# Optimization experiments

Measured on AMD Instinct MI355X. Metric: run time of the kernel, lower is better.

Reference implementation:

```python
import jax, jax.numpy as jnp
import numpy as np

EMB = 512       # emb_dim
H = 8           # n_heads
HD = EMB // H   # head_dim = 64
FREQ = 64       # freq_features
PERIOD = 0.1
N = 2048


def setup_inputs() -> dict:
    key = jax.random.key(0)
    ks = jax.random.split(key, 6)
    x = jax.random.normal(ks[0], (1, N, EMB), dtype=jnp.float32)
    v = jax.random.normal(ks[1], (1, N, 3), dtype=jnp.float32)
    vec_map = v / jnp.linalg.norm(v, axis=-1, keepdims=True)  # unit direction vectors
    s_in = 1.0 / np.sqrt(EMB)
    W_qkv = jax.random.normal(ks[2], (EMB, 3 * EMB), dtype=jnp.float32) * s_in
    b_qkv = jnp.zeros((3 * EMB,), dtype=jnp.float32)
    W_bias = jax.random.normal(ks[3], (FREQ, H), dtype=jnp.float32) * (1.0 / np.sqrt(FREQ))
    b_bias = jnp.zeros((H,), dtype=jnp.float32)
    W_out = jax.random.normal(ks[4], (EMB, EMB), dtype=jnp.float32) * s_in
    b_out = jnp.zeros((EMB,), dtype=jnp.float32)
    return {"x": x, "vec_map": vec_map, "W_qkv": W_qkv, "b_qkv": b_qkv,
            "W_bias": W_bias, "b_bias": b_bias, "W_out": W_out, "b_out": b_out}


def reference(x, vec_map, W_qkv, b_qkv, W_bias, b_bias, W_out, b_out):
    batch_dim = x.shape[:-2]
    n = x.shape[-2]
    # QKV projection -> (*, N, H, 3, HD)
    qkv = (x @ W_qkv + b_qkv).reshape(*batch_dim, n, H, 3, HD)
    q, k, v = (qkv[..., 0, :], qkv[..., 1, :], qkv[..., 2, :])
    # attention scores (*, Q, K, H), softmax over the K axis (axis=-2)
    attn = jnp.einsum('...qht,...kht->...qkh', q, k) / np.sqrt(HD)
    attn = jax.nn.softmax(attn, axis=-2)
    # relative bias from pairwise angles between direction vectors
    dot = jnp.einsum('...nc,...mc->...nm', vec_map, vec_map)
    angle = jnp.arccos(jnp.clip(dot, 0.0, 1.0)) / 0.001
    freqs = jnp.linspace(0.0, 1.0, FREQ // 2, dtype=jnp.float32) / PERIOD
    phase = freqs * angle[..., None]                      # (*, N, N, FREQ/2)
    pos = jnp.concatenate((jnp.sin(phase), jnp.cos(phase)), axis=-1)  # (*, N, N, FREQ)
    bias = pos @ W_bias + b_bias                          # (*, N, N, H)
    attn = attn + bias
    # weighted sum of values -> (*, N, EMB)
    y = jnp.einsum('...qkh,...kht->...qht', attn, v).reshape(*batch_dim, n, EMB)
    return y @ W_out + b_out
```

## Files before the change

kernel.cpp:

```cpp
#include <hip/hip_runtime.h>
#include <hip/hip_bf16.h>
#include <math.h>

#define NT 2048
#define EMBD 512
#define NH 8
#define QKV_LD 1536

typedef unsigned short u16;
typedef __attribute__((ext_vector_type(8))) short short8;
typedef __attribute__((ext_vector_type(4))) float v4f;

static __device__ __forceinline__ float bf2f(unsigned int u) {
    union { unsigned int i; float f; } c; c.i = u << 16; return c.f;
}
static __device__ __forceinline__ unsigned int f2bf(float x) {
    union { float f; unsigned int u; } c; c.f = x;
    return (c.u + 0x7fffu + ((c.u >> 16) & 1u)) >> 16;
}

__global__ __launch_bounds__(256) void split_x(const float* __restrict__ x,
    u16* __restrict__ xh, u16* __restrict__ xl)
{
    int i = (blockIdx.x * 256 + threadIdx.x) << 2;
    float4 v = *(const float4*)(x + i);
    float f[4] = {v.x, v.y, v.z, v.w};
    unsigned int hi[4], lo[4];
#pragma unroll
    for (int j = 0; j < 4; ++j) {
        hi[j] = f2bf(f[j]);
        lo[j] = f2bf(f[j] - bf2f(hi[j]));
    }
    uint2 wh; wh.x = hi[0] | (hi[1] << 16); wh.y = hi[2] | (hi[3] << 16);
    uint2 wl; wl.x = lo[0] | (lo[1] << 16); wl.y = lo[2] | (lo[3] << 16);
    *(uint2*)(xh + i) = wh;
    *(uint2*)(xl + i) = wl;
}

__global__ __launch_bounds__(256) void split_wt(const float* __restrict__ W,
    u16* __restrict__ wth, u16* __restrict__ wtl, int ld)
{
    __shared__ float tile[64][65];
    const int n0 = blockIdx.x << 6, k0 = blockIdx.y << 6;
    const int t = threadIdx.x;
    const int r = t >> 2, c4 = (t & 3) << 4;
#pragma unroll
    for (int j = 0; j < 4; ++j)
        *(float4*)&tile[r][c4 + (j << 2)] =
            *(const float4*)(W + (size_t)(k0 + r) * ld + n0 + c4 + (j << 2));
    __syncthreads();
    const int n_l = t >> 2;
    u16 th[16], tl[16];
#pragma unroll
    for (int j = 0; j < 16; ++j) {
        float f = tile[c4 + j][n_l];
        unsigned int h = f2bf(f);
        th[j] = (u16)h;
        tl[j] = (u16)f2bf(f - bf2f(h));
    }
    u16* dh = wth + (size_t)(n0 + n_l) * EMBD + k0 + c4;
    u16* dl = wtl + (size_t)(n0 + n_l) * EMBD + k0 + c4;
    *(uint4*)dh       = *(uint4*)&th[0];
    *(uint4*)(dh + 8) = *(uint4*)&th[8];
    *(uint4*)dl       = *(uint4*)&tl[0];
    *(uint4*)(dl + 8) = *(uint4*)&tl[8];
}

__global__ __launch_bounds__(256) void gemm_qkv_mfma(const u16* __restrict__ xh,
    const u16* __restrict__ xl, const u16* __restrict__ wth,
    const u16* __restrict__ wtl, const float* __restrict__ bias,
    u16* __restrict__ qkvb)
{
    const int n0 = blockIdx.x << 6, m0 = blockIdx.y << 6;
    const int w = threadIdx.x >> 6, lane = threadIdx.x & 63;
    const int wm = w >> 1, wn = w & 1;
    const int fr = lane & 15, kd = (lane >> 4) << 3;

    const u16* ah0 = xh + (size_t)(m0 + wm * 32 + fr) * EMBD + kd;
    const u16* al0 = xl + (size_t)(m0 + wm * 32 + fr) * EMBD + kd;
    const u16* bh0 = wth + (size_t)(n0 + wn * 32 + fr) * EMBD + kd;
    const u16* bl0 = wtl + (size_t)(n0 + wn * 32 + fr) * EMBD + kd;

    v4f acc[2][2] = {};
    for (int kc = 0; kc < EMBD; kc += 32) {
        short8 a_h[2], a_l[2], b_h[2], b_l[2];
#pragma unroll
        for (int im = 0; im < 2; ++im) {
            a_h[im] = *(const short8*)(ah0 + (size_t)im * 16 * EMBD + kc);
            a_l[im] = *(const short8*)(al0 + (size_t)im * 16 * EMBD + kc);
        }
#pragma unroll
        for (int in = 0; in < 2; ++in) {
            b_h[in] = *(const short8*)(bh0 + (size_t)in * 16 * EMBD + kc);
            b_l[in] = *(const short8*)(bl0 + (size_t)in * 16 * EMBD + kc);
        }
#pragma unroll
        for (int im = 0; im < 2; ++im)
#pragma unroll
            for (int in = 0; in < 2; ++in) {
                acc[im][in] = __builtin_amdgcn_mfma_f32_16x16x32_bf16(a_h[im], b_h[in], acc[im][in], 0, 0, 0);
                acc[im][in] = __builtin_amdgcn_mfma_f32_16x16x32_bf16(a_h[im], b_l[in], acc[im][in], 0, 0, 0);
                acc[im][in] = __builtin_amdgcn_mfma_f32_16x16x32_bf16(a_l[im], b_h[in], acc[im][in], 0, 0, 0);
            }
    }
    const int qr = (lane >> 4) << 2;
#pragma unroll
    for (int im = 0; im < 2; ++im)
#pragma unroll
        for (int in = 0; in < 2; ++in) {
            int n = n0 + wn * 32 + in * 16 + fr;
            float bv = bias[n];
#pragma unroll
            for (int r = 0; r < 4; ++r) {
                int m = m0 + wm * 32 + im * 16 + qr + r;
                qkvb[(size_t)m * QKV_LD + n] = (u16)f2bf(acc[im][in][r] + bv);
            }
        }
}

__global__ __launch_bounds__(256) void transpose_v(const u16* __restrict__ qkvb,
                                                   u16* __restrict__ Vt)
{
    __shared__ u16 tile[64][72];
    const int h = blockIdx.y, k0 = blockIdx.x << 6;
    const int t = threadIdx.x;
    {
        int r = t >> 2, cg = (t & 3) << 4;
        const u16* src = qkvb + (size_t)(k0 + r) * QKV_LD + h * 192 + 128 + cg;
        *(uint4*)&tile[r][cg]     = *(const uint4*)src;
        *(uint4*)&tile[r][cg + 8] = *(const uint4*)(src + 8);
    }
    __syncthreads();
    {
        int c = t >> 2, kg = (t & 3) << 4;
        u16 tmp[16];
#pragma unroll
        for (int j = 0; j < 16; ++j) tmp[j] = tile[kg + j][c];
        u16* dst = Vt + ((size_t)h * 64 + c) * NT + k0 + kg;
        *(uint4*)dst       = *(uint4*)&tmp[0];
        *(uint4*)(dst + 8) = *(uint4*)&tmp[8];
    }
}

__global__ __launch_bounds__(256) void flash_attn(const u16* __restrict__ qkvb,
    const u16* __restrict__ Vt, u16* __restrict__ nump,
    float* __restrict__ zpart)
{
    __shared__ u16 P[4][2][16][40];
    const int h = blockIdx.y, z = blockIdx.z;
    const int w = threadIdx.x >> 6, lane = threadIdx.x & 63;
    const int fr = lane & 15, kd = (lane >> 4) << 3, qr = (lane >> 4) << 2;
    const int q0 = (blockIdx.x << 6) + (w << 4);
    const int kbase = z << 9;

    const u16* qb = qkvb + (size_t)(q0 + fr) * QKV_LD + h * 192 + kd;
    short8 qa0 = *(const short8*)(qb);
    short8 qa1 = *(const short8*)(qb + 32);
    const u16* kbp = qkvb + (size_t)kbase * QKV_LD + h * 192 + 64 + kd;
    const u16* vb  = Vt + ((size_t)h * 64 + fr) * NT + kbase + kd;

    v4f acc[4] = {};
    float zac[4] = {};
    int buf = 0;
    for (int kt = 0; kt < 512; kt += 32) {
#pragma unroll
        for (int ks = 0; ks < 2; ++ks) {
            const u16* kr = kbp + (size_t)(kt + ks * 16 + fr) * QKV_LD;
            short8 kb0 = *(const short8*)(kr);
            short8 kb1 = *(const short8*)(kr + 32);
            v4f c = {};
            c = __builtin_amdgcn_mfma_f32_16x16x32_bf16(qa0, kb0, c, 0, 0, 0);
            c = __builtin_amdgcn_mfma_f32_16x16x32_bf16(qa1, kb1, c, 0, 0, 0);
#pragma unroll
            for (int r = 0; r < 4; ++r) {
                float ex = __expf(c[r] * 0.125f);
                zac[r] += ex;
                P[w][buf][qr + r][ks * 16 + fr] = (u16)f2bf(ex);
            }
        }
        union { uint2 u2[2]; short8 s8; } pa;
        pa.u2[0] = *(uint2*)&P[w][buf][fr][kd];
        pa.u2[1] = *(uint2*)&P[w][buf][fr][kd + 4];
#pragma unroll
        for (int ti = 0; ti < 4; ++ti) {
            short8 bfr = *(const short8*)(vb + (size_t)(ti * 16) * NT + kt);
            acc[ti] = __builtin_amdgcn_mfma_f32_16x16x32_bf16(pa.s8, bfr, acc[ti], 0, 0, 0);
        }
        buf ^= 1;
    }
#pragma unroll
    for (int off = 1; off < 16; off <<= 1)
#pragma unroll
        for (int r = 0; r < 4; ++r) zac[r] += __shfl_xor(zac[r], off);
    if (fr == 0) {
#pragma unroll
        for (int r = 0; r < 4; ++r)
            zpart[((size_t)z * NH + h) * NT + q0 + qr + r] = zac[r];
    }
    u16* np = nump + (size_t)z * NT * EMBD;
#pragma unroll
    for (int ti = 0; ti < 4; ++ti)
#pragma unroll
        for (int r = 0; r < 4; ++r)
            np[(size_t)(q0 + qr + r) * EMBD + (h << 6) + (ti << 4) + fr] =
                (u16)f2bf(acc[ti][r]);
}

__global__ __launch_bounds__(256) void bias_mat(const float* __restrict__ vec,
    const float* __restrict__ Wb, const float* __restrict__ bb,
    u16* __restrict__ bm)
{
    __shared__ float flds[32];
    __shared__ float vql[96], vkl[96];
    __shared__ float bbl[8];
    __shared__ float ang_lds[1057];
    __shared__ float biasl[8 * 1057];

    const int t = threadIdx.x;
    int b = blockIdx.x, tq = 0, rem = 64;
    while (b >= rem) { b -= rem; ++tq; --rem; }
    const int tk = tq + b;
    const int q0 = tq << 5, k0 = tk << 5;

    if (t < 32) flds[t] = __fdiv_rn(__fdiv_rn((float)t, 31.0f), 0.1f);
    else if (t < 128) vql[t - 32] = vec[q0 * 3 + (t - 32)];
    else if (t < 224) vkl[t - 128] = vec[k0 * 3 + (t - 128)];
    else if (t < 232) bbl[t - 224] = bb[t - 224];
    __syncthreads();

    {
        const int qq = t & 31, kb = (t >> 5) << 2;
        const float a0 = vql[qq * 3], a1 = vql[qq * 3 + 1], a2 = vql[qq * 3 + 2];
#pragma unroll
        for (int j = 0; j < 4; ++j) {
            const int kk = kb + j;
            float c0 = vkl[kk * 3], c1 = vkl[kk * 3 + 1], c2 = vkl[kk * 3 + 2];
            float dot = __fadd_rn(__fadd_rn(__fmul_rn(a0, c0), __fmul_rn(a1, c1)),
                                  __fmul_rn(a2, c2));
            float dotc = fminf(fmaxf(dot, 0.0f), 1.0f);
            ang_lds[qq * 33 + kk] = __fdiv_rn(acosf(dotc), 0.001f);
        }
    }
    __syncthreads();

    {
        const int w = t >> 6, lane = t & 63;
        const int fr = lane & 15, kd = (lane >> 4) << 3, qr = (lane >> 4) << 2;
        short8 BS, BC;
#pragma unroll
        for (int j = 0; j < 8; ++j) {
            float ws = (fr < 8) ? Wb[(kd + j) * 8 + fr] : 0.0f;
            float wc = (fr < 8) ? Wb[(32 + kd + j) * 8 + fr] : 0.0f;
            BS[j] = (short)f2bf(ws);
            BC[j] = (short)f2bf(wc);
        }
        for (int tt = w; tt < 64; tt += 4) {
            int p = (tt << 4) + fr;
            float ang = ang_lds[(p >> 5) * 33 + (p & 31)];
            short8 AS, AC;
#pragma unroll
            for (int j = 0; j < 8; ++j) {
                float ph = __fmul_rn(flds[kd + j], ang);
                float rv = ph * 0.15915494309189535f;
                float rf = rv - floorf(rv);
                AS[j] = (short)f2bf(__builtin_amdgcn_sinf(rf));
                AC[j] = (short)f2bf(__builtin_amdgcn_cosf(rf));
            }
            v4f c = {};
            c = __builtin_amdgcn_mfma_f32_16x16x32_bf16(AS, BS, c, 0, 0, 0);
            c = __builtin_amdgcn_mfma_f32_16x16x32_bf16(AC, BC, c, 0, 0, 0);
            if (fr < 8) {
#pragma unroll
                for (int r = 0; r < 4; ++r) {
                    int pp = (tt << 4) + qr + r;
                    biasl[fr * 1057 + (pp >> 5) * 33 + (pp & 31)] = c[r];
                }
            }
        }
    }
    __syncthreads();

    const int row = t >> 3, c4 = (t & 7) << 2;
#pragma unroll
    for (int h = 0; h < 8; ++h) {
        const float bv = bbl[h];
        unsigned int o[4];
#pragma unroll
        for (int j = 0; j < 4; ++j)
            o[j] = f2bf(biasl[h * 1057 + row * 33 + c4 + j] + bv);
        uint2 wv; wv.x = o[0] | (o[1] << 16); wv.y = o[2] | (o[3] << 16);
        *(uint2*)(bm + ((size_t)h * NT + q0 + row) * NT + k0 + c4) = wv;
    }
    if (tk != tq) {
#pragma unroll
        for (int h = 0; h < 8; ++h) {
            const float bv = bbl[h];
            unsigned int o[4];
#pragma unroll
            for (int j = 0; j < 4; ++j)
                o[j] = f2bf(biasl[h * 1057 + (c4 + j) * 33 + row] + bv);
            uint2 wv; wv.x = o[0] | (o[1] << 16); wv.y = o[2] | (o[3] << 16);
            *(uint2*)(bm + ((size_t)h * NT + k0 + row) * NT + q0 + c4) = wv;
        }
    }
}

__global__ __launch_bounds__(256) void biasv_mfma(const u16* __restrict__ bm,
    const u16* __restrict__ Vt, float* __restrict__ bpart)
{
    const int h = blockIdx.y, z = blockIdx.z;
    const int q0 = (blockIdx.x << 6) + ((threadIdx.x >> 6) << 4);
    const int lane = threadIdx.x & 63;
    const int fr = lane & 15;
    const int kd = (lane >> 4) << 3;
    const int kbase = z << 10;

    const u16* arow  = bm + (size_t)(h * NT + q0 + fr) * NT + kbase + kd;
    const u16* vbase = Vt + ((size_t)h * 64 + fr) * NT + kbase + kd;

    v4f c[4] = {};
    for (int ks = 0; ks < 1024; ks += 32) {
        short8 a = *(const short8*)(arow + ks);
#pragma unroll
        for (int nt = 0; nt < 4; ++nt) {
            short8 bv = *(const short8*)(vbase + (size_t)nt * 16 * NT + ks);
            c[nt] = __builtin_amdgcn_mfma_f32_16x16x32_bf16(a, bv, c[nt], 0, 0, 0);
        }
    }
    float* bp = bpart + (size_t)z * NT * EMBD;
    const int qr = (lane >> 4) << 2;
#pragma unroll
    for (int nt = 0; nt < 4; ++nt)
#pragma unroll
        for (int r = 0; r < 4; ++r)
            bp[(size_t)(q0 + qr + r) * EMBD + (h << 6) + (nt << 4) + fr] = c[nt][r];
}

__global__ __launch_bounds__(256) void combine_emit(const u16* __restrict__ nump,
    const float* __restrict__ zpart, const float* __restrict__ bpart,
    u16* __restrict__ yh, u16* __restrict__ yl)
{
    const int MN = NT * EMBD;
    int i = (blockIdx.x * 256 + threadIdx.x) << 2;
    const int q = i >> 9, h = (i & 511) >> 6;
    float zs = 0.f;
#pragma unroll
    for (int z = 0; z < 4; ++z) zs += zpart[((size_t)z * NH + h) * NT + q];
    const float inv = 1.0f / zs;
    float a[4] = {};
#pragma unroll
    for (int z = 0; z < 4; ++z) {
        uint2 r = *(const uint2*)(nump + (size_t)z * MN + i);
        a[0] += bf2f(r.x & 0xffffu); a[1] += bf2f(r.x >> 16);
        a[2] += bf2f(r.y & 0xffffu); a[3] += bf2f(r.y >> 16);
    }
    float bsum[4] = {};
#pragma unroll
    for (int z = 0; z < 2; ++z) {
        float4 p = *(const float4*)(bpart + (size_t)z * MN + i);
        bsum[0] += p.x; bsum[1] += p.y; bsum[2] += p.z; bsum[3] += p.w;
    }
    unsigned int hi[4], lo[4];
#pragma unroll
    for (int j = 0; j < 4; ++j) {
        float y = a[j] * inv + bsum[j];
        hi[j] = f2bf(y);
        lo[j] = f2bf(y - bf2f(hi[j]));
    }
    uint2 wh; wh.x = hi[0] | (hi[1] << 16); wh.y = hi[2] | (hi[3] << 16);
    uint2 wl; wl.x = lo[0] | (lo[1] << 16); wl.y = lo[2] | (lo[3] << 16);
    *(uint2*)(yh + i) = wh;
    *(uint2*)(yl + i) = wl;
}

__global__ __launch_bounds__(256) void gemm_out_mfma(const u16* __restrict__ yh,
    const u16* __restrict__ yl, const u16* __restrict__ wh,
    const u16* __restrict__ wl, const float* __restrict__ bias,
    float* __restrict__ out)
{
    const int n0 = blockIdx.x << 6, m0 = blockIdx.y << 6;
    const int w = threadIdx.x >> 6, lane = threadIdx.x & 63;
    const int wm = w >> 1, wn = w & 1;
    const int fr = lane & 15, kd = (lane >> 4) << 3;

    const u16* ah0 = yh + (size_t)(m0 + wm * 32 + fr) * EMBD + kd;
    const u16* al0 = yl + (size_t)(m0 + wm * 32 + fr) * EMBD + kd;
    const u16* bh0 = wh + (size_t)(n0 + wn * 32 + fr) * EMBD + kd;
    const u16* bl0 = wl + (size_t)(n0 + wn * 32 + fr) * EMBD + kd;

    v4f acc[2][2] = {};
    for (int kc = 0; kc < EMBD; kc += 32) {
        short8 a_h[2], a_l[2], b_h[2], b_l[2];
#pragma unroll
        for (int im = 0; im < 2; ++im) {
            a_h[im] = *(const short8*)(ah0 + (size_t)im * 16 * EMBD + kc);
            a_l[im] = *(const short8*)(al0 + (size_t)im * 16 * EMBD + kc);
        }
#pragma unroll
        for (int in = 0; in < 2; ++in) {
            b_h[in] = *(const short8*)(bh0 + (size_t)in * 16 * EMBD + kc);
            b_l[in] = *(const short8*)(bl0 + (size_t)in * 16 * EMBD + kc);
        }
#pragma unroll
        for (int im = 0; im < 2; ++im)
#pragma unroll
            for (int in = 0; in < 2; ++in) {
                acc[im][in] = __builtin_amdgcn_mfma_f32_16x16x32_bf16(a_h[im], b_h[in], acc[im][in], 0, 0, 0);
                acc[im][in] = __builtin_amdgcn_mfma_f32_16x16x32_bf16(a_h[im], b_l[in], acc[im][in], 0, 0, 0);
                acc[im][in] = __builtin_amdgcn_mfma_f32_16x16x32_bf16(a_l[im], b_h[in], acc[im][in], 0, 0, 0);
            }
    }
    const int qr = (lane >> 4) << 2;
#pragma unroll
    for (int im = 0; im < 2; ++im)
#pragma unroll
        for (int in = 0; in < 2; ++in) {
            int n = n0 + wn * 32 + in * 16 + fr;
            float bv = bias[n];
#pragma unroll
            for (int r = 0; r < 4; ++r) {
                int m = m0 + wm * 32 + im * 16 + qr + r;
                out[(size_t)m * EMBD + n] = acc[im][in][r] + bv;
            }
        }
}

extern "C" void kernel_launch(void* const* d_in, const int* in_sizes, int n_in,
                              void* d_out, int out_size, void* d_ws, size_t ws_size,
                              hipStream_t stream)
{
    const float* x    = (const float*)d_in[0];
    const float* vec  = (const float*)d_in[1];
    const float* Wqkv = (const float*)d_in[2];
    const float* bqkv = (const float*)d_in[3];
    const float* Wb   = (const float*)d_in[4];
    const float* bb   = (const float*)d_in[5];
    const float* Wout = (const float*)d_in[6];
    const float* bout = (const float*)d_in[7];
    float* out = (float*)d_out;

    char* ws = (char*)d_ws;
    u16*   qkvb  = (u16*)(ws);
    u16*   Vt    = (u16*)(ws + 6291456);
    float* zpart = (float*)(ws + 8388608);
    u16*   nump  = (u16*)(ws + 8650752);
    float* bpart = (float*)(ws + 17039360);
    u16*   yh    = (u16*)(ws + 25427968);
    u16*   yl    = (u16*)(ws + 27525120);
    u16*   bm    = (u16*)(ws + 29622272);
    u16*   xh    = (u16*)(ws + 29622272);
    u16*   xl    = (u16*)(ws + 31719424);
    u16*   wth   = (u16*)(ws + 33816576);
    u16*   wtl   = (u16*)(ws + 35389440);
    u16*   woth  = (u16*)(ws + 29622272);
    u16*   wotl  = (u16*)(ws + 30146560);

    split_x<<<1024, 256, 0, stream>>>(x, xh, xl);
    split_wt<<<dim3(24, 8), 256, 0, stream>>>(Wqkv, wth, wtl, QKV_LD);
    gemm_qkv_mfma<<<dim3(24, 32), 256, 0, stream>>>(xh, xl, wth, wtl, bqkv, qkvb);
    transpose_v<<<dim3(32, 8), 256, 0, stream>>>(qkvb, Vt);
    flash_attn<<<dim3(32, 8, 4), 256, 0, stream>>>(qkvb, Vt, nump, zpart);
    bias_mat<<<2080, 256, 0, stream>>>(vec, Wb, bb, bm);
    biasv_mfma<<<dim3(32, 8, 2), 256, 0, stream>>>(bm, Vt, bpart);
    combine_emit<<<1024, 256, 0, stream>>>(nump, zpart, bpart, yh, yl);
    split_wt<<<dim3(8, 8), 256, 0, stream>>>(Wout, woth, wotl, EMBD);
    gemm_out_mfma<<<dim3(8, 32), 256, 0, stream>>>(yh, yl, woth, wotl, bout, out);
}
```

Baseline: 283.8 us.

## Merge prep kernels, split flash attention over more key chunks, prefetch K

Folds the x split and both weight split/transposes into one prep launch, removing two kernel launches. Flash attention now splits keys into 8 chunks of 256 instead of 4 of 512, doubling grid parallelism, and prefetches the next K tile while using a single P buffer. The bias-times-V kernel is unrolled to two MFMAs per step. The workspace is reorganised so nump aliases the big scratch region after bias_mat/biasv finish, which is why flash_attn is reordered after biasv. In exchange, combine_emit reads twice as many partial sums.

```diff
diff --git a/kernel.cpp b/kernel.cpp
--- a/kernel.cpp
+++ b/kernel.cpp
@@ -19,30 +19,10 @@
     return (c.u + 0x7fffu + ((c.u >> 16) & 1u)) >> 16;
 }
 
-__global__ __launch_bounds__(256) void split_x(const float* __restrict__ x,
-    u16* __restrict__ xh, u16* __restrict__ xl)
-{
-    int i = (blockIdx.x * 256 + threadIdx.x) << 2;
-    float4 v = *(const float4*)(x + i);
-    float f[4] = {v.x, v.y, v.z, v.w};
-    unsigned int hi[4], lo[4];
-#pragma unroll
-    for (int j = 0; j < 4; ++j) {
-        hi[j] = f2bf(f[j]);
-        lo[j] = f2bf(f[j] - bf2f(hi[j]));
-    }
-    uint2 wh; wh.x = hi[0] | (hi[1] << 16); wh.y = hi[2] | (hi[3] << 16);
-    uint2 wl; wl.x = lo[0] | (lo[1] << 16); wl.y = lo[2] | (lo[3] << 16);
-    *(uint2*)(xh + i) = wh;
-    *(uint2*)(xl + i) = wl;
-}
-
-__global__ __launch_bounds__(256) void split_wt(const float* __restrict__ W,
-    u16* __restrict__ wth, u16* __restrict__ wtl, int ld)
+static __device__ __forceinline__ void split_wt_tile(const float* __restrict__ W,
+    u16* __restrict__ wth, u16* __restrict__ wtl, int ld, int n0, int k0, int t)
 {
     __shared__ float tile[64][65];
-    const int n0 = blockIdx.x << 6, k0 = blockIdx.y << 6;
-    const int t = threadIdx.x;
     const int r = t >> 2, c4 = (t & 3) << 4;
 #pragma unroll
     for (int j = 0; j < 4; ++j)
@@ -64,6 +44,36 @@
     *(uint4*)(dh + 8) = *(uint4*)&th[8];
     *(uint4*)dl       = *(uint4*)&tl[0];
     *(uint4*)(dl + 8) = *(uint4*)&tl[8];
+}
+
+__global__ __launch_bounds__(256) void prep(const float* __restrict__ x,
+    const float* __restrict__ Wqkv, const float* __restrict__ Wout,
+    u16* __restrict__ xh, u16* __restrict__ xl,
+    u16* __restrict__ wth, u16* __restrict__ wtl,
+    u16* __restrict__ woth, u16* __restrict__ wotl)
+{
+    const int b = blockIdx.x, t = threadIdx.x;
+    if (b < 1024) {
+        int i = (b * 256 + t) << 2;
+        float4 v = *(const float4*)(x + i);
+        float f[4] = {v.x, v.y, v.z, v.w};
+        unsigned int hi[4], lo[4];
+#pragma unroll
+        for (int j = 0; j < 4; ++j) {
+            hi[j] = f2bf(f[j]);
+            lo[j] = f2bf(f[j] - bf2f(hi[j]));
+        }
+        uint2 wh; wh.x = hi[0] | (hi[1] << 16); wh.y = hi[2] | (hi[3] << 16);
+        uint2 wl; wl.x = lo[0] | (lo[1] << 16); wl.y = lo[2] | (lo[3] << 16);
+        *(uint2*)(xh + i) = wh;
+        *(uint2*)(xl + i) = wl;
+    } else if (b < 1216) {
+        int bb = b - 1024;
+        split_wt_tile(Wqkv, wth, wtl, QKV_LD, (bb % 24) << 6, (bb / 24) << 6, t);
+    } else {
+        int bb = b - 1216;
+        split_wt_tile(Wout, woth, wotl, EMBD, (bb & 7) << 6, (bb >> 3) << 6, t);
+    }
 }
 
 __global__ __launch_bounds__(256) void gemm_qkv_mfma(const u16* __restrict__ xh,
@@ -142,70 +152,6 @@
     }
 }
 
-__global__ __launch_bounds__(256) void flash_attn(const u16* __restrict__ qkvb,
-    const u16* __restrict__ Vt, u16* __restrict__ nump,
-    float* __restrict__ zpart)
-{
-    __shared__ u16 P[4][2][16][40];
-    const int h = blockIdx.y, z = blockIdx.z;
-    const int w = threadIdx.x >> 6, lane = threadIdx.x & 63;
-    const int fr = lane & 15, kd = (lane >> 4) << 3, qr = (lane >> 4) << 2;
-    const int q0 = (blockIdx.x << 6) + (w << 4);
-    const int kbase = z << 9;
-
-    const u16* qb = qkvb + (size_t)(q0 + fr) * QKV_LD + h * 192 + kd;
-    short8 qa0 = *(const short8*)(qb);
-    short8 qa1 = *(const short8*)(qb + 32);
-    const u16* kbp = qkvb + (size_t)kbase * QKV_LD + h * 192 + 64 + kd;
-    const u16* vb  = Vt + ((size_t)h * 64 + fr) * NT + kbase + kd;
-
-    v4f acc[4] = {};
-    float zac[4] = {};
-    int buf = 0;
-    for (int kt = 0; kt < 512; kt += 32) {
-#pragma unroll
-        for (int ks = 0; ks < 2; ++ks) {
-            const u16* kr = kbp + (size_t)(kt + ks * 16 + fr) * QKV_LD;
-            short8 kb0 = *(const short8*)(kr);
-            short8 kb1 = *(const short8*)(kr + 32);
-            v4f c = {};
-            c = __builtin_amdgcn_mfma_f32_16x16x32_bf16(qa0, kb0, c, 0, 0, 0);
-            c = __builtin_amdgcn_mfma_f32_16x16x32_bf16(qa1, kb1, c, 0, 0, 0);
-#pragma unroll
-            for (int r = 0; r < 4; ++r) {
-                float ex = __expf(c[r] * 0.125f);
-                zac[r] += ex;
-                P[w][buf][qr + r][ks * 16 + fr] = (u16)f2bf(ex);
-            }
-        }
-        union { uint2 u2[2]; short8 s8; } pa;
-        pa.u2[0] = *(uint2*)&P[w][buf][fr][kd];
-        pa.u2[1] = *(uint2*)&P[w][buf][fr][kd + 4];
-#pragma unroll
-        for (int ti = 0; ti < 4; ++ti) {
-            short8 bfr = *(const short8*)(vb + (size_t)(ti * 16) * NT + kt);
-            acc[ti] = __builtin_amdgcn_mfma_f32_16x16x32_bf16(pa.s8, bfr, acc[ti], 0, 0, 0);
-        }
-        buf ^= 1;
-    }
-#pragma unroll
-    for (int off = 1; off < 16; off <<= 1)
-#pragma unroll
-        for (int r = 0; r < 4; ++r) zac[r] += __shfl_xor(zac[r], off);
-    if (fr == 0) {
-#pragma unroll
-        for (int r = 0; r < 4; ++r)
-            zpart[((size_t)z * NH + h) * NT + q0 + qr + r] = zac[r];
-    }
-    u16* np = nump + (size_t)z * NT * EMBD;
-#pragma unroll
-    for (int ti = 0; ti < 4; ++ti)
-#pragma unroll
-        for (int r = 0; r < 4; ++r)
-            np[(size_t)(q0 + qr + r) * EMBD + (h << 6) + (ti << 4) + fr] =
-                (u16)f2bf(acc[ti][r]);
-}
-
 __global__ __launch_bounds__(256) void bias_mat(const float* __restrict__ vec,
     const float* __restrict__ Wb, const float* __restrict__ bb,
     u16* __restrict__ bm)
@@ -319,12 +265,15 @@
     const u16* vbase = Vt + ((size_t)h * 64 + fr) * NT + kbase + kd;
 
     v4f c[4] = {};
-    for (int ks = 0; ks < 1024; ks += 32) {
-        short8 a = *(const short8*)(arow + ks);
+    for (int ks = 0; ks < 1024; ks += 64) {
+        short8 a0 = *(const short8*)(arow + ks);
+        short8 a1 = *(const short8*)(arow + ks + 32);
 #pragma unroll
         for (int nt = 0; nt < 4; ++nt) {
-            short8 bv = *(const short8*)(vbase + (size_t)nt * 16 * NT + ks);
-            c[nt] = __builtin_amdgcn_mfma_f32_16x16x32_bf16(a, bv, c[nt], 0, 0, 0);
+            short8 b0 = *(const short8*)(vbase + (size_t)nt * 16 * NT + ks);
+            short8 b1 = *(const short8*)(vbase + (size_t)nt * 16 * NT + ks + 32);
+            c[nt] = __builtin_amdgcn_mfma_f32_16x16x32_bf16(a0, b0, c[nt], 0, 0, 0);
+            c[nt] = __builtin_amdgcn_mfma_f32_16x16x32_bf16(a1, b1, c[nt], 0, 0, 0);
         }
     }
     float* bp = bpart + (size_t)z * NT * EMBD;
@@ -334,6 +283,83 @@
 #pragma unroll
         for (int r = 0; r < 4; ++r)
             bp[(size_t)(q0 + qr + r) * EMBD + (h << 6) + (nt << 4) + fr] = c[nt][r];
+}
+
+__global__ __launch_bounds__(256) void flash_attn(const u16* __restrict__ qkvb,
+    const u16* __restrict__ Vt, u16* __restrict__ nump,
+    float* __restrict__ zpart)
+{
+    __shared__ u16 P[4][16][40];
+    const int h = blockIdx.y, z = blockIdx.z;
+    const int w = threadIdx.x >> 6, lane = threadIdx.x & 63;
+    const int fr = lane & 15, kd = (lane >> 4) << 3, qr = (lane >> 4) << 2;
+    const int q0 = (blockIdx.x << 6) + (w << 4);
+    const int kbase = z << 8;
+
+    const u16* qb = qkvb + (size_t)(q0 + fr) * QKV_LD + h * 192 + kd;
+    short8 qa0 = *(const short8*)(qb);
+    short8 qa1 = *(const short8*)(qb + 32);
+    const u16* kbp = qkvb + (size_t)kbase * QKV_LD + h * 192 + 64 + kd;
+    const u16* vb  = Vt + ((size_t)h * 64 + fr) * NT + kbase + kd;
+
+    short8 k0a, k0b, k1a, k1b;
+    {
+        const u16* kr0 = kbp + (size_t)fr * QKV_LD;
+        const u16* kr1 = kbp + (size_t)(16 + fr) * QKV_LD;
+        k0a = *(const short8*)(kr0); k0b = *(const short8*)(kr0 + 32);
+        k1a = *(const short8*)(kr1); k1b = *(const short8*)(kr1 + 32);
+    }
+    v4f acc[4] = {};
+    float zac[4] = {};
+    for (int kt = 0; kt < 256; kt += 32) {
+        short8 ck0a = k0a, ck0b = k0b, ck1a = k1a, ck1b = k1b;
+        if (kt + 32 < 256) {
+            const u16* kr0 = kbp + (size_t)(kt + 32 + fr) * QKV_LD;
+            const u16* kr1 = kbp + (size_t)(kt + 48 + fr) * QKV_LD;
+            k0a = *(const short8*)(kr0); k0b = *(const short8*)(kr0 + 32);
+            k1a = *(const short8*)(kr1); k1b = *(const short8*)(kr1 + 32);
+        }
+        short8 v0 = *(const short8*)(vb + (size_t)0 * 16 * NT + kt);
+        short8 v1 = *(const short8*)(vb + (size_t)1 * 16 * NT + kt);
+        short8 v2 = *(const short8*)(vb + (size_t)2 * 16 * NT + kt);
+        short8 v3 = *(const short8*)(vb + (size_t)3 * 16 * NT + kt);
+        v4f c0 = {}, c1 = {};
+        c0 = __builtin_amdgcn_mfma_f32_16x16x32_bf16(qa0, ck0a, c0, 0, 0, 0);
+        c0 = __builtin_amdgcn_mfma_f32_16x16x32_bf16(qa1, ck0b, c0, 0, 0, 0);
+        c1 = __builtin_amdgcn_mfma_f32_16x16x32_bf16(qa0, ck1a, c1, 0, 0, 0);
+        c1 = __builtin_amdgcn_mfma_f32_16x16x32_bf16(qa1, ck1b, c1, 0, 0, 0);
+#pragma unroll
+        for (int r = 0; r < 4; ++r) {
+            float e0 = __expf(c0[r] * 0.125f);
+            float e1 = __expf(c1[r] * 0.125f);
+            zac[r] += e0 + e1;
+            P[w][qr + r][fr]      = (u16)f2bf(e0);
+            P[w][qr + r][16 + fr] = (u16)f2bf(e1);
+        }
+        union { uint2 u2[2]; short8 s8; } pa;
+        pa.u2[0] = *(uint2*)&P[w][fr][kd];
+        pa.u2[1] = *(uint2*)&P[w][fr][kd + 4];
+        acc[0] = __builtin_amdgcn_mfma_f32_16x16x32_bf16(pa.s8, v0, acc[0], 0, 0, 0);
+        acc[1] = __builtin_amdgcn_mfma_f32_16x16x32_bf16(pa.s8, v1, acc[1], 0, 0, 0);
+        acc[2] = __builtin_amdgcn_mfma_f32_16x16x32_bf16(pa.s8, v2, acc[2], 0, 0, 0);
+        acc[3] = __builtin_amdgcn_mfma_f32_16x16x32_bf16(pa.s8, v3, acc[3], 0, 0, 0);
+    }
+#pragma unroll
+    for (int off = 1; off < 16; off <<= 1)
+#pragma unroll
+        for (int r = 0; r < 4; ++r) zac[r] += __shfl_xor(zac[r], off);
+    if (fr == 0) {
+#pragma unroll
+        for (int r = 0; r < 4; ++r)
+            zpart[((size_t)z * NH + h) * NT + q0 + qr + r] = zac[r];
+    }
+    u16* np = nump + (size_t)z * NT * EMBD;
+#pragma unroll
+    for (int ti = 0; ti < 4; ++ti)
+#pragma unroll
+        for (int r = 0; r < 4; ++r)
+            np[(size_t)(q0 + qr + r) * EMBD + (h << 6) + (ti << 4) + fr] =
+                (u16)f2bf(acc[ti][r]);
 }
 
 __global__ __launch_bounds__(256) void combine_emit(const u16* __restrict__ nump,
@@ -345,11 +371,11 @@
     const int q = i >> 9, h = (i & 511) >> 6;
     float zs = 0.f;
 #pragma unroll
-    for (int z = 0; z < 4; ++z) zs += zpart[((size_t)z * NH + h) * NT + q];
+    for (int z = 0; z < 8; ++z) zs += zpart[((size_t)z * NH + h) * NT + q];
     const float inv = 1.0f / zs;
     float a[4] = {};
 #pragma unroll
-    for (int z = 0; z < 4; ++z) {
+    for (int z = 0; z < 8; ++z) {
         uint2 r = *(const uint2*)(nump + (size_t)z * MN + i);
         a[0] += bf2f(r.x & 0xffffu); a[1] += bf2f(r.x >> 16);
         a[2] += bf2f(r.y & 0xffffu); a[3] += bf2f(r.y >> 16);
@@ -443,26 +469,25 @@
     u16*   qkvb  = (u16*)(ws);
     u16*   Vt    = (u16*)(ws + 6291456);
     float* zpart = (float*)(ws + 8388608);
-    u16*   nump  = (u16*)(ws + 8650752);
-    float* bpart = (float*)(ws + 17039360);
-    u16*   yh    = (u16*)(ws + 25427968);
-    u16*   yl    = (u16*)(ws + 27525120);
-    u16*   bm    = (u16*)(ws + 29622272);
-    u16*   xh    = (u16*)(ws + 29622272);
-    u16*   xl    = (u16*)(ws + 31719424);
-    u16*   wth   = (u16*)(ws + 33816576);
-    u16*   wtl   = (u16*)(ws + 35389440);
-    u16*   woth  = (u16*)(ws + 29622272);
-    u16*   wotl  = (u16*)(ws + 30146560);
-
-    split_x<<<1024, 256, 0, stream>>>(x, xh, xl);
-    split_wt<<<dim3(24, 8), 256, 0, stream>>>(Wqkv, wth, wtl, QKV_LD);
+    float* bpart = (float*)(ws + 8912896);
+    u16*   yh    = (u16*)(ws + 17301504);
+    u16*   yl    = (u16*)(ws + 19398656);
+    u16*   woth  = (u16*)(ws + 21495808);
+    u16*   wotl  = (u16*)(ws + 22020096);
+    char*  big   = ws + 22544384;
+    u16*   xh    = (u16*)(big);
+    u16*   xl    = (u16*)(big + 2097152);
+    u16*   wth   = (u16*)(big + 4194304);
+    u16*   wtl   = (u16*)(big + 5767168);
+    u16*   bm    = (u16*)(big);
+    u16*   nump  = (u16*)(big);
+
+    prep<<<1280, 256, 0, stream>>>(x, Wqkv, Wout, xh, xl, wth, wtl, woth, wotl);
     gemm_qkv_mfma<<<dim3(24, 32), 256, 0, stream>>>(xh, xl, wth, wtl, bqkv, qkvb);
     transpose_v<<<dim3(32, 8), 256, 0, stream>>>(qkvb, Vt);
-    flash_attn<<<dim3(32, 8, 4), 256, 0, stream>>>(qkvb, Vt, nump, zpart);
     bias_mat<<<2080, 256, 0, stream>>>(vec, Wb, bb, bm);
     biasv_mfma<<<dim3(32, 8, 2), 256, 0, stream>>>(bm, Vt, bpart);
+    flash_attn<<<dim3(32, 8, 8), 256, 0, stream>>>(qkvb, Vt, nump, zpart);
     combine_emit<<<1024, 256, 0, stream>>>(nump, zpart, bpart, yh, yl);
-    split_wt<<<dim3(8, 8), 256, 0, stream>>>(Wout, woth, wotl, EMBD);
     gemm_out_mfma<<<dim3(8, 32), 256, 0, stream>>>(yh, yl, woth, wotl, bout, out);
 }
```

Result: no change. 284.4 us (+0.2%).

## Merge prep kernels, fuse V transpose into QKV GEMM, resplit bias-V reduction

Applied to the files above, without the earlier changes.

One prep kernel now splits x, W_qkv and W_out into bf16 hi/lo pairs, replacing three separate launches. The QKV GEMM blocks that produce V tiles stage them in LDS and write the transposed Vt directly, so the standalone transpose kernel is gone. bias_mat stores bf16 into a smaller LDS buffer and folds the bias into the MFMA accumulator init. biasv_mfma now splits K four ways with two MFMAs per step, and combine_emit sums four partials. The workspace is reordered so bm and nump share one buffer, which requires the bias pass to run before flash attention and moves launch order around.

```diff
diff --git a/kernel.cpp b/kernel.cpp
--- a/kernel.cpp
+++ b/kernel.cpp
@@ -19,30 +19,10 @@
     return (c.u + 0x7fffu + ((c.u >> 16) & 1u)) >> 16;
 }
 
-__global__ __launch_bounds__(256) void split_x(const float* __restrict__ x,
-    u16* __restrict__ xh, u16* __restrict__ xl)
-{
-    int i = (blockIdx.x * 256 + threadIdx.x) << 2;
-    float4 v = *(const float4*)(x + i);
-    float f[4] = {v.x, v.y, v.z, v.w};
-    unsigned int hi[4], lo[4];
-#pragma unroll
-    for (int j = 0; j < 4; ++j) {
-        hi[j] = f2bf(f[j]);
-        lo[j] = f2bf(f[j] - bf2f(hi[j]));
-    }
-    uint2 wh; wh.x = hi[0] | (hi[1] << 16); wh.y = hi[2] | (hi[3] << 16);
-    uint2 wl; wl.x = lo[0] | (lo[1] << 16); wl.y = lo[2] | (lo[3] << 16);
-    *(uint2*)(xh + i) = wh;
-    *(uint2*)(xl + i) = wl;
-}
-
-__global__ __launch_bounds__(256) void split_wt(const float* __restrict__ W,
-    u16* __restrict__ wth, u16* __restrict__ wtl, int ld)
+static __device__ __forceinline__ void split_wt_tile(const float* __restrict__ W,
+    u16* __restrict__ wth, u16* __restrict__ wtl, int ld, int n0, int k0, int t)
 {
     __shared__ float tile[64][65];
-    const int n0 = blockIdx.x << 6, k0 = blockIdx.y << 6;
-    const int t = threadIdx.x;
     const int r = t >> 2, c4 = (t & 3) << 4;
 #pragma unroll
     for (int j = 0; j < 4; ++j)
@@ -66,13 +46,46 @@
     *(uint4*)(dl + 8) = *(uint4*)&tl[8];
 }
 
+__global__ __launch_bounds__(256) void prep(const float* __restrict__ x,
+    const float* __restrict__ Wqkv, const float* __restrict__ Wout,
+    u16* __restrict__ xh, u16* __restrict__ xl,
+    u16* __restrict__ wth, u16* __restrict__ wtl,
+    u16* __restrict__ woth, u16* __restrict__ wotl)
+{
+    const int b = blockIdx.x, t = threadIdx.x;
+    if (b < 1024) {
+        int i = (b * 256 + t) << 2;
+        float4 v = *(const float4*)(x + i);
+        float f[4] = {v.x, v.y, v.z, v.w};
+        unsigned int hi[4], lo[4];
+#pragma unroll
+        for (int j = 0; j < 4; ++j) {
+            hi[j] = f2bf(f[j]);
+            lo[j] = f2bf(f[j] - bf2f(hi[j]));
+        }
+        uint2 wh; wh.x = hi[0] | (hi[1] << 16); wh.y = hi[2] | (hi[3] << 16);
+        uint2 wl; wl.x = lo[0] | (lo[1] << 16); wl.y = lo[2] | (lo[3] << 16);
+        *(uint2*)(xh + i) = wh;
+        *(uint2*)(xl + i) = wl;
+    } else if (b < 1216) {
+        int bb = b - 1024;
+        split_wt_tile(Wqkv, wth, wtl, QKV_LD, (bb % 24) << 6, (bb / 24) << 6, t);
+    } else {
+        int bb = b - 1216;
+        split_wt_tile(Wout, woth, wotl, EMBD, (bb & 7) << 6, (bb >> 3) << 6, t);
+    }
+}
+
 __global__ __launch_bounds__(256) void gemm_qkv_mfma(const u16* __restrict__ xh,
     const u16* __restrict__ xl, const u16* __restrict__ wth,
     const u16* __restrict__ wtl, const float* __restrict__ bias,
-    u16* __restrict__ qkvb)
-{
-    const int n0 = blockIdx.x << 6, m0 = blockIdx.y << 6;
-    const int w = threadIdx.x >> 6, lane = threadIdx.x & 63;
+    u16* __restrict__ qkvb, u16* __restrict__ Vt)
+{
+    __shared__ u16 vtile[64][72];
+    const int bn = blockIdx.x;
+    const int n0 = bn << 6, m0 = blockIdx.y << 6;
+    const int t = threadIdx.x;
+    const int w = t >> 6, lane = t & 63;
     const int wm = w >> 1, wn = w & 1;
     const int fr = lane & 15, kd = (lane >> 4) << 3;
 
@@ -104,42 +117,173 @@
             }
     }
     const int qr = (lane >> 4) << 2;
-#pragma unroll
-    for (int im = 0; im < 2; ++im)
-#pragma unroll
-        for (int in = 0; in < 2; ++in) {
-            int n = n0 + wn * 32 + in * 16 + fr;
-            float bv = bias[n];
-#pragma unroll
-            for (int r = 0; r < 4; ++r) {
-                int m = m0 + wm * 32 + im * 16 + qr + r;
-                qkvb[(size_t)m * QKV_LD + n] = (u16)f2bf(acc[im][in][r] + bv);
-            }
-        }
-}
-
-__global__ __launch_bounds__(256) void transpose_v(const u16* __restrict__ qkvb,
-                                                   u16* __restrict__ Vt)
-{
-    __shared__ u16 tile[64][72];
-    const int h = blockIdx.y, k0 = blockIdx.x << 6;
-    const int t = threadIdx.x;
-    {
-        int r = t >> 2, cg = (t & 3) << 4;
-        const u16* src = qkvb + (size_t)(k0 + r) * QKV_LD + h * 192 + 128 + cg;
-        *(uint4*)&tile[r][cg]     = *(const uint4*)src;
-        *(uint4*)&tile[r][cg + 8] = *(const uint4*)(src + 8);
-    }
-    __syncthreads();
-    {
-        int c = t >> 2, kg = (t & 3) << 4;
+    if (bn % 3 != 2) {
+#pragma unroll
+        for (int im = 0; im < 2; ++im)
+#pragma unroll
+            for (int in = 0; in < 2; ++in) {
+                int n = n0 + wn * 32 + in * 16 + fr;
+                float bv = bias[n];
+#pragma unroll
+                for (int r = 0; r < 4; ++r) {
+                    int m = m0 + wm * 32 + im * 16 + qr + r;
+                    qkvb[(size_t)m * QKV_LD + n] = (u16)f2bf(acc[im][in][r] + bv);
+                }
+            }
+    } else {
+        const int h = bn / 3;
+#pragma unroll
+        for (int im = 0; im < 2; ++im)
+#pragma unroll
+            for (int in = 0; in < 2; ++in) {
+                int nl = wn * 32 + in * 16 + fr;
+                float bv = bias[n0 + nl];
+#pragma unroll
+                for (int r = 0; r < 4; ++r)
+                    vtile[wm * 32 + im * 16 + qr + r][nl] =
+                        (u16)f2bf(acc[im][in][r] + bv);
+            }
+        __syncthreads();
+        const int c = t >> 2, kg = (t & 3) << 4;
         u16 tmp[16];
 #pragma unroll
-        for (int j = 0; j < 16; ++j) tmp[j] = tile[kg + j][c];
-        u16* dst = Vt + ((size_t)h * 64 + c) * NT + k0 + kg;
+        for (int j = 0; j < 16; ++j) tmp[j] = vtile[kg + j][c];
+        u16* dst = Vt + ((size_t)h * 64 + c) * NT + m0 + kg;
         *(uint4*)dst       = *(uint4*)&tmp[0];
         *(uint4*)(dst + 8) = *(uint4*)&tmp[8];
     }
+}
+
+__global__ __launch_bounds__(256) void bias_mat(const float* __restrict__ vec,
+    const float* __restrict__ Wb, const float* __restrict__ bb,
+    u16* __restrict__ bm)
+{
+    __shared__ float flds[32];
+    __shared__ float vql[96], vkl[96];
+    __shared__ float bbl[8];
+    __shared__ float ang_lds[1057];
+    __shared__ u16 biaslu[8 * 1057];
+
+    const int t = threadIdx.x;
+    int b = blockIdx.x, tq = 0, rem = 64;
+    while (b >= rem) { b -= rem; ++tq; --rem; }
+    const int tk = tq + b;
+    const int q0 = tq << 5, k0 = tk << 5;
+
+    if (t < 32) flds[t] = __fdiv_rn(__fdiv_rn((float)t, 31.0f), 0.1f);
+    else if (t < 128) vql[t - 32] = vec[q0 * 3 + (t - 32)];
+    else if (t < 224) vkl[t - 128] = vec[k0 * 3 + (t - 128)];
+    else if (t < 232) bbl[t - 224] = bb[t - 224];
+    __syncthreads();
+
+    {
+        const int qq = t & 31, kb = (t >> 5) << 2;
+        const float a0 = vql[qq * 3], a1 = vql[qq * 3 + 1], a2 = vql[qq * 3 + 2];
+#pragma unroll
+        for (int j = 0; j < 4; ++j) {
+            const int kk = kb + j;
+            float c0 = vkl[kk * 3], c1 = vkl[kk * 3 + 1], c2 = vkl[kk * 3 + 2];
+            float dot = __fadd_rn(__fadd_rn(__fmul_rn(a0, c0), __fmul_rn(a1, c1)),
+                                  __fmul_rn(a2, c2));
+            float dotc = fminf(fmaxf(dot, 0.0f), 1.0f);
+            ang_lds[qq * 33 + kk] = __fdiv_rn(acosf(dotc), 0.001f);
+        }
+    }
+    __syncthreads();
+
+    {
+        const int w = t >> 6, lane = t & 63;
+        const int fr = lane & 15, kd = (lane >> 4) << 3, qr = (lane >> 4) << 2;
+        short8 BS, BC;
+#pragma unroll
+        for (int j = 0; j < 8; ++j) {
+            float ws = (fr < 8) ? Wb[(kd + j) * 8 + fr] : 0.0f;
+            float wc = (fr < 8) ? Wb[(32 + kd + j) * 8 + fr] : 0.0f;
+            BS[j] = (short)f2bf(ws);
+            BC[j] = (short)f2bf(wc);
+        }
+        const float bb0 = (fr < 8) ? bbl[fr] : 0.0f;
+        for (int tt = w; tt < 64; tt += 4) {
+            int p = (tt << 4) + fr;
+            float ang = ang_lds[(p >> 5) * 33 + (p & 31)];
+            short8 AS, AC;
+#pragma unroll
+            for (int j = 0; j < 8; ++j) {
+                float ph = __fmul_rn(flds[kd + j], ang);
+                float rv = ph * 0.15915494309189535f;
+                float rf = rv - floorf(rv);
+                AS[j] = (short)f2bf(__builtin_amdgcn_sinf(rf));
+                AC[j] = (short)f2bf(__builtin_amdgcn_cosf(rf));
+            }
+            v4f c = {bb0, bb0, bb0, bb0};
+            c = __builtin_amdgcn_mfma_f32_16x16x32_bf16(AS, BS, c, 0, 0, 0);
+            c = __builtin_amdgcn_mfma_f32_16x16x32_bf16(AC, BC, c, 0, 0, 0);
+            if (fr < 8) {
+#pragma unroll
+                for (int r = 0; r < 4; ++r) {
+                    int pp = (tt << 4) + qr + r;
+                    biaslu[fr * 1057 + (pp >> 5) * 33 + (pp & 31)] = (u16)f2bf(c[r]);
+                }
+            }
+        }
+    }
+    __syncthreads();
+
+    const int row = t >> 3, c4 = (t & 7) << 2;
+#pragma unroll
+    for (int h = 0; h < 8; ++h) {
+        unsigned int o[4];
+#pragma unroll
+        for (int j = 0; j < 4; ++j)
+            o[j] = biaslu[h * 1057 + row * 33 + c4 + j];
+        uint2 wv; wv.x = o[0] | (o[1] << 16); wv.y = o[2] | (o[3] << 16);
+        *(uint2*)(bm + ((size_t)h * NT + q0 + row) * NT + k0 + c4) = wv;
+    }
+    if (tk != tq) {
+#pragma unroll
+        for (int h = 0; h < 8; ++h) {
+            unsigned int o[4];
+#pragma unroll
+            for (int j = 0; j < 4; ++j)
+                o[j] = biaslu[h * 1057 + (c4 + j) * 33 + row];
+            uint2 wv; wv.x = o[0] | (o[1] << 16); wv.y = o[2] | (o[3] << 16);
+            *(uint2*)(bm + ((size_t)h * NT + k0 + row) * NT + q0 + c4) = wv;
+        }
+    }
+}
+
+__global__ __launch_bounds__(256) void biasv_mfma(const u16* __restrict__ bm,
+    const u16* __restrict__ Vt, float* __restrict__ bpart)
+{
+    const int h = blockIdx.y, z = blockIdx.z;
+    const int q0 = (blockIdx.x << 6) + ((threadIdx.x >> 6) << 4);
+    const int lane = threadIdx.x & 63;
+    const int fr = lane & 15;
+    const int kd = (lane >> 4) << 3;
+    const int kbase = z << 9;
+
+    const u16* arow  = bm + (size_t)(h * NT + q0 + fr) * NT + kbase + kd;
+    const u16* vbase = Vt + ((size_t)h * 64 + fr) * NT + kbase + kd;
+
+    v4f c[4] = {};
+    for (int ks = 0; ks < 512; ks += 64) {
+        short8 a0 = *(const short8*)(arow + ks);
+        short8 a1 = *(const short8*)(arow + ks + 32);
+#pragma unroll
+        for (int nt = 0; nt < 4; ++nt) {
+            short8 b0 = *(const short8*)(vbase + (size_t)nt * 16 * NT + ks);
+            short8 b1 = *(const short8*)(vbase + (size_t)nt * 16 * NT + ks + 32);
+            c[nt] = __builtin_amdgcn_mfma_f32_16x16x32_bf16(a0, b0, c[nt], 0, 0, 0);
+            c[nt] = __builtin_amdgcn_mfma_f32_16x16x32_bf16(a1, b1, c[nt], 0, 0, 0);
+        }
+    }
+    float* bp = bpart + (size_t)z * NT * EMBD;
+    const int qr = (lane >> 4) << 2;
+#pragma unroll
+    for (int nt = 0; nt < 4; ++nt)
+#pragma unroll
+        for (int r = 0; r < 4; ++r)
+            bp[(size_t)(q0 + qr + r) * EMBD + (h << 6) + (nt << 4) + fr] = c[nt][r];
 }
 
 __global__ __launch_bounds__(256) void flash_attn(const u16* __restrict__ qkvb,
@@ -206,136 +350,6 @@
                 (u16)f2bf(acc[ti][r]);
 }
 
-__global__ __launch_bounds__(256) void bias_mat(const float* __restrict__ vec,
-    const float* __restrict__ Wb, const float* __restrict__ bb,
-    u16* __restrict__ bm)
-{
-    __shared__ float flds[32];
-    __shared__ float vql[96], vkl[96];
-    __shared__ float bbl[8];
-    __shared__ float ang_lds[1057];
-    __shared__ float biasl[8 * 1057];
-
-    const int t = threadIdx.x;
-    int b = blockIdx.x, tq = 0, rem = 64;
-    while (b >= rem) { b -= rem; ++tq; --rem; }
-    const int tk = tq + b;
-    const int q0 = tq << 5, k0 = tk << 5;
-
-    if (t < 32) flds[t] = __fdiv_rn(__fdiv_rn((float)t, 31.0f), 0.1f);
-    else if (t < 128) vql[t - 32] = vec[q0 * 3 + (t - 32)];
-    else if (t < 224) vkl[t - 128] = vec[k0 * 3 + (t - 128)];
-    else if (t < 232) bbl[t - 224] = bb[t - 224];
-    __syncthreads();
-
-    {
-        const int qq = t & 31, kb = (t >> 5) << 2;
-        const float a0 = vql[qq * 3], a1 = vql[qq * 3 + 1], a2 = vql[qq * 3 + 2];
-#pragma unroll
-        for (int j = 0; j < 4; ++j) {
-            const int kk = kb + j;
-            float c0 = vkl[kk * 3], c1 = vkl[kk * 3 + 1], c2 = vkl[kk * 3 + 2];
-            float dot = __fadd_rn(__fadd_rn(__fmul_rn(a0, c0), __fmul_rn(a1, c1)),
-                                  __fmul_rn(a2, c2));
-            float dotc = fminf(fmaxf(dot, 0.0f), 1.0f);
-            ang_lds[qq * 33 + kk] = __fdiv_rn(acosf(dotc), 0.001f);
-        }
-    }
-    __syncthreads();
-
-    {
-        const int w = t >> 6, lane = t & 63;
-        const int fr = lane & 15, kd = (lane >> 4) << 3, qr = (lane >> 4) << 2;
-        short8 BS, BC;
-#pragma unroll
-        for (int j = 0; j < 8; ++j) {
-            float ws = (fr < 8) ? Wb[(kd + j) * 8 + fr] : 0.0f;
-            float wc = (fr < 8) ? Wb[(32 + kd + j) * 8 + fr] : 0.0f;
-            BS[j] = (short)f2bf(ws);
-            BC[j] = (short)f2bf(wc);
-        }
-        for (int tt = w; tt < 64; tt += 4) {
-            int p = (tt << 4) + fr;
-            float ang = ang_lds[(p >> 5) * 33 + (p & 31)];
-            short8 AS, AC;
-#pragma unroll
-            for (int j = 0; j < 8; ++j) {
-                float ph = __fmul_rn(flds[kd + j], ang);
-                float rv = ph * 0.15915494309189535f;
-                float rf = rv - floorf(rv);
-                AS[j] = (short)f2bf(__builtin_amdgcn_sinf(rf));
-                AC[j] = (short)f2bf(__builtin_amdgcn_cosf(rf));
-            }
-            v4f c = {};
-            c = __builtin_amdgcn_mfma_f32_16x16x32_bf16(AS, BS, c, 0, 0, 0);
-            c = __builtin_amdgcn_mfma_f32_16x16x32_bf16(AC, BC, c, 0, 0, 0);
-            if (fr < 8) {
-#pragma unroll
-                for (int r = 0; r < 4; ++r) {
-                    int pp = (tt << 4) + qr + r;
-                    biasl[fr * 1057 + (pp >> 5) * 33 + (pp & 31)] = c[r];
-                }
-            }
-        }
-    }
-    __syncthreads();
-
-    const int row = t >> 3, c4 = (t & 7) << 2;
-#pragma unroll
-    for (int h = 0; h < 8; ++h) {
-        const float bv = bbl[h];
-        unsigned int o[4];
-#pragma unroll
-        for (int j = 0; j < 4; ++j)
-            o[j] = f2bf(biasl[h * 1057 + row * 33 + c4 + j] + bv);
-        uint2 wv; wv.x = o[0] | (o[1] << 16); wv.y = o[2] | (o[3] << 16);
-        *(uint2*)(bm + ((size_t)h * NT + q0 + row) * NT + k0 + c4) = wv;
-    }
-    if (tk != tq) {
-#pragma unroll
-        for (int h = 0; h < 8; ++h) {
-            const float bv = bbl[h];
-            unsigned int o[4];
-#pragma unroll
-            for (int j = 0; j < 4; ++j)
-                o[j] = f2bf(biasl[h * 1057 + (c4 + j) * 33 + row] + bv);
-            uint2 wv; wv.x = o[0] | (o[1] << 16); wv.y = o[2] | (o[3] << 16);
-            *(uint2*)(bm + ((size_t)h * NT + k0 + row) * NT + q0 + c4) = wv;
-        }
-    }
-}
-
-__global__ __launch_bounds__(256) void biasv_mfma(const u16* __restrict__ bm,
-    const u16* __restrict__ Vt, float* __restrict__ bpart)
-{
-    const int h = blockIdx.y, z = blockIdx.z;
-    const int q0 = (blockIdx.x << 6) + ((threadIdx.x >> 6) << 4);
-    const int lane = threadIdx.x & 63;
-    const int fr = lane & 15;
-    const int kd = (lane >> 4) << 3;
-    const int kbase = z << 10;
-
-    const u16* arow  = bm + (size_t)(h * NT + q0 + fr) * NT + kbase + kd;
-    const u16* vbase = Vt + ((size_t)h * 64 + fr) * NT + kbase + kd;
-
-    v4f c[4] = {};
-    for (int ks = 0; ks < 1024; ks += 32) {
-        short8 a = *(const short8*)(arow + ks);
-#pragma unroll
-        for (int nt = 0; nt < 4; ++nt) {
-            short8 bv = *(const short8*)(vbase + (size_t)nt * 16 * NT + ks);
-            c[nt] = __builtin_amdgcn_mfma_f32_16x16x32_bf16(a, bv, c[nt], 0, 0, 0);
-        }
-    }
-    float* bp = bpart + (size_t)z * NT * EMBD;
-    const int qr = (lane >> 4) << 2;
-#pragma unroll
-    for (int nt = 0; nt < 4; ++nt)
-#pragma unroll
-        for (int r = 0; r < 4; ++r)
-            bp[(size_t)(q0 + qr + r) * EMBD + (h << 6) + (nt << 4) + fr] = c[nt][r];
-}
-
 __global__ __launch_bounds__(256) void combine_emit(const u16* __restrict__ nump,
     const float* __restrict__ zpart, const float* __restrict__ bpart,
     u16* __restrict__ yh, u16* __restrict__ yl)
@@ -356,7 +370,7 @@
     }
     float bsum[4] = {};
 #pragma unroll
-    for (int z = 0; z < 2; ++z) {
+    for (int z = 0; z < 4; ++z) {
         float4 p = *(const float4*)(bpart + (size_t)z * MN + i);
         bsum[0] += p.x; bsum[1] += p.y; bsum[2] += p.z; bsum[3] += p.w;
     }
@@ -443,26 +457,24 @@
     u16*   qkvb  = (u16*)(ws);
     u16*   Vt    = (u16*)(ws + 6291456);
     float* zpart = (float*)(ws + 8388608);
-    u16*   nump  = (u16*)(ws + 8650752);
-    float* bpart = (float*)(ws + 17039360);
+    float* bpart = (float*)(ws + 8650752);
     u16*   yh    = (u16*)(ws + 25427968);
     u16*   yl    = (u16*)(ws + 27525120);
-    u16*   bm    = (u16*)(ws + 29622272);
-    u16*   xh    = (u16*)(ws + 29622272);
-    u16*   xl    = (u16*)(ws + 31719424);
-    u16*   wth   = (u16*)(ws + 33816576);
-    u16*   wtl   = (u16*)(ws + 35389440);
     u16*   woth  = (u16*)(ws + 29622272);
     u16*   wotl  = (u16*)(ws + 30146560);
-
-    split_x<<<1024, 256, 0, stream>>>(x, xh, xl);
-    split_wt<<<dim3(24, 8), 256, 0, stream>>>(Wqkv, wth, wtl, QKV_LD);
-    gemm_qkv_mfma<<<dim3(24, 32), 256, 0, stream>>>(xh, xl, wth, wtl, bqkv, qkvb);
-    transpose_v<<<dim3(32, 8), 256, 0, stream>>>(qkvb, Vt);
+    char*  big   = ws + 30670848;
+    u16*   xh    = (u16*)(big);
+    u16*   xl    = (u16*)(big + 2097152);
+    u16*   wth   = (u16*)(big + 4194304);
+    u16*   wtl   = (u16*)(big + 5767168);
+    u16*   bm    = (u16*)(big);
+    u16*   nump  = (u16*)(big);
+
+    prep<<<1280, 256, 0, stream>>>(x, Wqkv, Wout, xh, xl, wth, wtl, woth, wotl);
+    gemm_qkv_mfma<<<dim3(24, 32), 256, 0, stream>>>(xh, xl, wth, wtl, bqkv, qkvb, Vt);
+    bias_mat<<<2080, 256, 0, stream>>>(vec, Wb, bb, bm);
+    biasv_mfma<<<dim3(32, 8, 4), 256, 0, stream>>>(bm, Vt, bpart);
     flash_attn<<<dim3(32, 8, 4), 256, 0, stream>>>(qkvb, Vt, nump, zpart);
-    bias_mat<<<2080, 256, 0, stream>>>(vec, Wb, bb, bm);
-    biasv_mfma<<<dim3(32, 8, 2), 256, 0, stream>>>(bm, Vt, bpart);
     combine_emit<<<1024, 256, 0, stream>>>(nump, zpart, bpart, yh, yl);
-    split_wt<<<dim3(8, 8), 256, 0, stream>>>(Wout, woth, wotl, EMBD);
     gemm_out_mfma<<<dim3(8, 32), 256, 0, stream>>>(yh, yl, woth, wotl, bout, out);
 }
```

Result: no change. 281.9 us (-0.7%).
